# Kernel tuning notes

Measured on AMD Instinct MI355X. Metric: run time of the kernel, lower is better.

## Reference

```python
import jax, jax.numpy as jnp
import numpy as np

B, HIMG, WIMG = 8, 24, 24
WIDTH, NCH, CW = 1024, 8, 128
NHEADS, HD = 8, 16
HALF = HD // 2
NFREQ, VOCAB, NCLS = 32, 256, 10
HIDDEN = 4096
EPS = 1e-6
LAMBDA_INIT = 0.8 - 0.6 * float(np.exp(-0.3 * 0.0))  # layer_idx = 0


def rmsnorm(x, w, eps=EPS):
    return x * jax.lax.rsqrt(jnp.mean(x * x, axis=-1, keepdims=True) + eps) * w


def causal_attn(q, k, v, scale):
    # q,k: [B,H,L,d2], v: [B,H,L,D]
    L = q.shape[2]
    scores = jnp.einsum('bhqd,bhkd->bhqk', q, k) * scale
    mask = jnp.tril(jnp.ones((L, L), dtype=bool))
    scores = jnp.where(mask, scores, -jnp.inf)
    return jnp.einsum('bhqk,bhkd->bhqd', jax.nn.softmax(scores, axis=-1), v)


def diff_attn(h, qkv_w, qkv_b, qn_w, kn_w, hn_w, lq1, lk1, lq2, lk2, ow, ob):
    Bb, L, C = h.shape
    qkv = jax.nn.silu(h @ qkv_w + qkv_b).reshape(Bb, L, 3, NHEADS, HD)
    q, k, v = qkv[:, :, 0], qkv[:, :, 1], qkv[:, :, 2]
    t = lambda a: a.transpose(0, 2, 1, 3)  # [B,L,H,d] -> [B,H,L,d]
    q1 = t(rmsnorm(q[..., :HALF], qn_w)); q2 = t(rmsnorm(q[..., HALF:], qn_w))
    k1 = t(rmsnorm(k[..., :HALF], kn_w)); k2 = t(rmsnorm(k[..., HALF:], kn_w))
    v = t(v)
    lam = jnp.exp(jnp.dot(lq1, lk1)) - jnp.exp(jnp.dot(lq2, lk2)) + LAMBDA_INIT
    scale = 1.0 / np.sqrt(HALF)
    out1 = causal_attn(q1, k1, v, scale)
    out2 = causal_attn(q2, k2, v, scale)
    diff = rmsnorm(out1 - lam * out2, hn_w) * (1.0 - LAMBDA_INIT)
    out = diff.transpose(0, 2, 1, 3).reshape(Bb, L, C)
    return jax.nn.silu(out @ ow + ob)


def setup_inputs() -> dict:
    key = jax.random.key(0)
    ks = iter(jax.random.split(key, 64))
    n = lambda shape, s=0.02: jax.random.normal(next(ks), shape, jnp.float32) * s
    return dict(
        x=jax.random.uniform(next(ks), (B, HIMG, WIMG), jnp.float32),
        top_k=4,
        pixel_embed=n((VOCAB, WIDTH)),
        freq_h=n((NFREQ,), 0.1), freq_w=n((NFREQ,), 0.1),
        phase_h=jnp.zeros((NFREQ,), jnp.float32), phase_w=jnp.zeros((NFREQ,), jnp.float32),
        pos_proj_w=n((4 * NFREQ, WIDTH)), pos_proj_b=jnp.zeros((WIDTH,), jnp.float32),
        embed_norm_w=jnp.ones((WIDTH,), jnp.float32),
        se_w1=n((WIDTH, WIDTH // 4)), se_b1=jnp.zeros((WIDTH // 4,), jnp.float32),
        se_w2=n((WIDTH // 4, WIDTH)), se_b2=jnp.zeros((WIDTH,), jnp.float32),
        mix_norm_w=jnp.ones((WIDTH,), jnp.float32),
        mlp_w1=n((WIDTH, HIDDEN)), mlp_b1=jnp.zeros((HIDDEN,), jnp.float32),
        mlp_w2=n((HIDDEN, WIDTH)), mlp_b2=jnp.zeros((WIDTH,), jnp.float32),
        mlp_norm_w=jnp.ones((WIDTH,), jnp.float32),
        router_w=n((WIDTH, NCH)), router_b=jnp.zeros((NCH,), jnp.float32),
        qkv_w=n((NCH, CW, 3 * CW)), qkv_b=jnp.zeros((NCH, 3 * CW), jnp.float32),
        q_norm_w=jnp.ones((NCH, HALF), jnp.float32), k_norm_w=jnp.ones((NCH, HALF), jnp.float32),
        head_norm_w=jnp.ones((NCH, HD), jnp.float32),
        lam_q1=n((NCH, HALF), 0.1), lam_k1=n((NCH, HALF), 0.1),
        lam_q2=n((NCH, HALF), 0.1), lam_k2=n((NCH, HALF), 0.1),
        out_w=n((NCH, CW, CW)), out_b=jnp.zeros((NCH, CW), jnp.float32),
        seg_norm_w=jnp.ones((NCH, CW), jnp.float32),
        head_w=n((WIDTH, NCLS)), head_b=jnp.zeros((NCLS,), jnp.float32),
    )


def reference(x, top_k, pixel_embed, freq_h, freq_w, phase_h, phase_w, pos_proj_w,
              pos_proj_b, embed_norm_w, se_w1, se_b1, se_w2, se_b2, mix_norm_w,
              mlp_w1, mlp_b1, mlp_w2, mlp_b2, mlp_norm_w, router_w, router_b,
              qkv_w, qkv_b, q_norm_w, k_norm_w, head_norm_w, lam_q1, lam_k1,
              lam_q2, lam_k2, out_w, out_b, seg_norm_w, head_w, head_b):
    Bb, H, W = x.shape
    L = H * W
    # LearnedSinusoidal2DEmbed
    hp = jnp.arange(H, dtype=jnp.float32) / H
    wp = jnp.arange(W, dtype=jnp.float32) / W
    fh = jax.nn.softplus(freq_h) * 10.0
    fw = jax.nn.softplus(freq_w) * 10.0
    ha = hp[:, None] * fh + phase_h          # [H, NFREQ]
    wa = wp[:, None] * fw + phase_w
    h_enc = jnp.concatenate([jnp.sin(ha), jnp.cos(ha)], -1)
    w_enc = jnp.concatenate([jnp.sin(wa), jnp.cos(wa)], -1)
    pos = jnp.concatenate([jnp.broadcast_to(h_enc[:, None], (H, W, 2 * NFREQ)),
                           jnp.broadcast_to(w_enc[None, :], (H, W, 2 * NFREQ))], -1)
    pos = pos @ pos_proj_w + pos_proj_b      # [H, W, WIDTH]
    xi = jnp.clip((x * 255.0).astype(jnp.int32), 0, 255).reshape(Bb, L)
    h = pixel_embed[xi] + pos.reshape(1, L, WIDTH)
    h = rmsnorm(h, embed_norm_w)
    # ChannelMixer: SE + RMSNorm residual, MLP residual, top-k router
    s = jnp.mean(h, axis=1)
    s = jax.nn.sigmoid(jax.nn.silu(s @ se_w1 + se_b1) @ se_w2 + se_b2)
    h = h + rmsnorm(h * s[:, None, :] - h, mix_norm_w)
    h = h + rmsnorm(jax.nn.silu(h @ mlp_w1 + mlp_b1) @ mlp_w2 + mlp_b2, mlp_norm_w)
    logits_r = jnp.mean(h, axis=1) @ router_w + router_b   # [B, NCH]
    tv, ti = jax.lax.top_k(logits_r, top_k)
    rw = jnp.zeros_like(logits_r).at[jnp.arange(Bb)[:, None], ti].set(jax.nn.softmax(tv, axis=-1))
    # ChannelSegment: per-channel differential attention expert, routed
    outs = []
    for i in range(NCH):
        hi = h[..., i * CW:(i + 1) * CW]
        o = diff_attn(hi, qkv_w[i], qkv_b[i], q_norm_w[i], k_norm_w[i], head_norm_w[i],
                      lam_q1[i], lam_k1[i], lam_q2[i], lam_k2[i], out_w[i], out_b[i])
        hi = hi + rmsnorm(o, seg_norm_w[i])
        outs.append(hi * rw[:, i][:, None, None])
    h = jnp.concatenate(outs, axis=-1)
    # classifier head
    return jnp.mean(h, axis=1) @ head_w + head_b
```

## Files before the change

kernel.cpp:

```cpp
#include <hip/hip_runtime.h>
#include <math.h>

typedef __bf16 bf16;
typedef __bf16 bf16x8 __attribute__((ext_vector_type(8)));
typedef __bf16 bf16x4 __attribute__((ext_vector_type(4)));
typedef __bf16 bf16x2 __attribute__((ext_vector_type(2)));
typedef float f32x4 __attribute__((ext_vector_type(4)));
typedef short s16x4 __attribute__((ext_vector_type(4)));

constexpr int Bsz = 8, HIMG = 24, WIMG = 24;
constexpr int Lq = 576;
constexpr int WIDTH = 1024, NCH = 8, CW = 128;
constexpr int NHEADS = 8, HD = 16, HALF = 8;
constexpr float EPS = 1e-6f;
constexpr float LAMINIT = 0.2f;
constexpr float QSCALE_E = 0.35355339059327373f * 1.4426950408889634f;
constexpr int ROWS = Bsz * Lq;
constexpr long PSTRIDE = 4718592;

__device__ __forceinline__ float fexp2(float x) {
#if __has_builtin(__builtin_amdgcn_exp2f)
  return __builtin_amdgcn_exp2f(x);
#else
  return exp2f(x);
#endif
}

constexpr size_t B_HB    = 0;
constexpr size_t B_G2B   = B_HB    + 9437184;
constexpr size_t B_ENCB  = B_G2B   + 9437184;
constexpr size_t B_POSWT = B_ENCB  + 163840;
constexpr size_t B_QKVWT = B_POSWT + 262144;
constexpr size_t B_OWT   = B_QKVWT + 786432;
constexpr size_t B_SE    = B_OWT   + 262144;
constexpr size_t B_T1    = B_SE    + 32768;
constexpr size_t B_MP    = B_T1    + 8192;
constexpr size_t B_RW    = B_MP    + 524288;
constexpr size_t B_LAM   = B_RW    + 256;
constexpr size_t B_POOL  = B_LAM   + 256;
constexpr size_t WS_BIG  = B_POOL + 8388608 + 8388608 + 37748736;
constexpr size_t WS_BIG2 = WS_BIG + 9437184;
constexpr size_t WS_BIG3 = WS_BIG + 4 * 9437184;

__device__ __forceinline__ float blockReduceSum256(float v, float* red) {
  #pragma unroll
  for (int off = 32; off; off >>= 1) v += __shfl_down(v, off, 64);
  int lane = threadIdx.x & 63, wid = threadIdx.x >> 6;
  if (lane == 0) red[wid] = v;
  __syncthreads();
  float total = 0.f;
  #pragma unroll
  for (int i = 0; i < 4; i++) total += red[i];
  return total;
}
__device__ __forceinline__ float silu(float x) { return x / (1.f + __expf(-x)); }

__device__ __forceinline__ void gl16(const bf16* g, bf16* l) {
  __builtin_amdgcn_global_load_lds(
      (const __attribute__((address_space(1))) void*)g,
      (__attribute__((address_space(3))) void*)l, 16, 0, 0);
}

__device__ __forceinline__ f32x4 mfma16(bf16x4 a, bf16x4 b, f32x4 c) {
#if __has_builtin(__builtin_amdgcn_mfma_f32_16x16x16bf16_1k)
  union { bf16x4 h; s16x4 s; } ua, ub;
  ua.h = a; ub.h = b;
  return __builtin_amdgcn_mfma_f32_16x16x16bf16_1k(ua.s, ub.s, c, 0, 0, 0);
#else
  f32x4 d = c;
  asm volatile("v_mfma_f32_16x16x16_bf16 %0, %1, %2, %0"
               : "+v"(d) : "v"(a), "v"(b));
  return d;
#endif
}

__device__ __forceinline__ void tcast_tile(const float* __restrict__ W,
    bf16* __restrict__ Wt, int K, int N, long zo, int bx, int by) {
  __shared__ float t[32][33];
  int n0 = bx * 32, k0 = by * 32;
  int tid = threadIdx.x;
  int r = tid >> 3, c4 = (tid & 7) * 4;
  const float4 v = *(const float4*)(W + zo + (long)(k0 + r) * N + n0 + c4);
  t[c4 + 0][r] = v.x; t[c4 + 1][r] = v.y; t[c4 + 2][r] = v.z; t[c4 + 3][r] = v.w;
  __syncthreads();
  bf16* dst = Wt + zo + (long)(n0 + r) * K + k0 + c4;
  dst[0] = (bf16)t[r][c4 + 0]; dst[1] = (bf16)t[r][c4 + 1];
  dst[2] = (bf16)t[r][c4 + 2]; dst[3] = (bf16)t[r][c4 + 3];
}

__global__ __launch_bounds__(256) void k_tcast_all(
    const float* __restrict__ w1, const float* __restrict__ w2,
    const float* __restrict__ posw, const float* __restrict__ qkvw,
    const float* __restrict__ outw,
    bf16* __restrict__ W1T, bf16* __restrict__ W2T, bf16* __restrict__ POSWT,
    bf16* __restrict__ QKVWT, bf16* __restrict__ OWT) {
  int bid = blockIdx.x;
  if (bid < 4096) {
    tcast_tile(w1, W1T, 1024, 4096, 0, bid % 128, bid / 128);
  } else if (bid < 8192) {
    int t = bid - 4096;
    tcast_tile(w2, W2T, 4096, 1024, 0, t % 32, t / 32);
  } else if (bid < 8320) {
    int t = bid - 8192;
    tcast_tile(posw, POSWT, 128, 1024, 0, t % 32, t / 32);
  } else if (bid < 8704) {
    int t = bid - 8320;
    int z = t / 48; t -= z * 48;
    tcast_tile(qkvw, QKVWT, 128, 384, (long)z * 49152, t % 12, t / 12);
  } else {
    int t = bid - 8704;
    int z = t / 16; t -= z * 16;
    tcast_tile(outw, OWT, 128, 128, (long)z * 16384, t % 4, t / 4);
  }
}

__global__ void k_enc_b(const float* __restrict__ fh, const float* __restrict__ fw,
                        const float* __restrict__ ph, const float* __restrict__ pw,
                        bf16* __restrict__ enc) {
  int idx = blockIdx.x * blockDim.x + threadIdx.x;
  if (idx >= Lq * 128) return;
  int l = idx >> 7, c = idx & 127;
  int hh = l / WIMG, ww = l % WIMG;
  float v;
  if (c < 64) {
    int f = c & 31;
    float fr = log1pf(__expf(fh[f])) * 10.f;
    float a = (hh / (float)HIMG) * fr + ph[f];
    v = (c < 32) ? sinf(a) : cosf(a);
  } else {
    int f = c & 31;
    float fr = log1pf(__expf(fw[f])) * 10.f;
    float a = (ww / (float)WIMG) * fr + pw[f];
    v = (c < 96) ? sinf(a) : cosf(a);
  }
  enc[idx] = (bf16)v;
}

template <int ACT, int OUTBF, int SWZ>
__global__ __launch_bounds__(256) void gemm_bt(
    const bf16* __restrict__ A, int lda, long aZs,
    const bf16* __restrict__ Bt, int ldb, long bZs,
    const float* __restrict__ bias, int biasZs,
    void* __restrict__ Cv, int ldc, long cZs,
    int M, int N, int K) {
  __shared__ bf16 As[128 * 32];
  __shared__ bf16 Bs[128 * 32];
  int tid = threadIdx.x;
  int m0, n0, z;
  if constexpr (SWZ == 0) {
    m0 = blockIdx.y * 128; n0 = blockIdx.x * 128; z = blockIdx.z;
  } else if constexpr (SWZ == 1) {
    int lid = blockIdx.x;
    int xcd = lid & 7, idx = lid >> 3;
    int j = idx & 15, G = xcd + 8 * (idx >> 4);
    m0 = (G % 36) * 128; n0 = ((G / 36) * 16 + j) * 128; z = 0;
  } else {
    int lid = blockIdx.x;
    int xcd = lid & 7, idx = lid >> 3;
    int n = idx & 7, G = xcd + 8 * (idx >> 3);
    m0 = (G % 36) * 128; n0 = n * 128; z = G / 36;
  }
  const bf16* Ab = A + (long)z * aZs;
  const bf16* Bb = Bt + (long)z * bZs;
  f32x4 acc[4][4] = {};
  int wv = tid >> 6, lane = tid & 63;
  int wrow = (wv >> 1) * 64, wcol = (wv & 1) * 64;
  int lm = lane & 15, lq = lane >> 4;
  const bf16* ag = Ab + (long)(m0 + (tid >> 2)) * lda + (tid & 3) * 8;
  const bf16* bg = Bb + (long)(n0 + (tid >> 2)) * ldb + (tid & 3) * 8;
  bf16* asd = As + tid * 8;
  bf16* bsd = Bs + tid * 8;
  for (int k0 = 0; k0 < K; k0 += 32) {
    gl16(ag + k0, asd);
    gl16(ag + k0 + 64L * lda, asd + 2048);
    gl16(bg + k0, bsd);
    gl16(bg + k0 + 64L * ldb, bsd + 2048);
    __syncthreads();
    bf16x8 af[4], bfr[4];
    #pragma unroll
    for (int i = 0; i < 4; i++) {
      af[i]  = *(const bf16x8*)(As + (wrow + i * 16 + lm) * 32 + lq * 8);
      bfr[i] = *(const bf16x8*)(Bs + (wcol + i * 16 + lm) * 32 + lq * 8);
    }
    #pragma unroll
    for (int i = 0; i < 4; i++)
      #pragma unroll
      for (int j = 0; j < 4; j++)
        acc[i][j] = __builtin_amdgcn_mfma_f32_16x16x32_bf16(af[i], bfr[j], acc[i][j], 0, 0, 0);
    __syncthreads();
  }
  long cz = (long)z * cZs;
  const float* bz = bias ? bias + (long)z * biasZs : nullptr;
  #pragma unroll
  for (int i = 0; i < 4; i++) {
    int row = m0 + wrow + i * 16 + lq * 4;
    #pragma unroll
    for (int j = 0; j < 4; j++) {
      int col = n0 + wcol + j * 16 + lm;
      float bv = bz ? bz[col] : 0.f;
      #pragma unroll
      for (int r = 0; r < 4; r++) {
        float v = acc[i][j][r] + bv;
        if (ACT == 1) v = silu(v);
        long off = cz + (long)(row + r) * ldc + col;
        if (OUTBF) ((bf16*)Cv)[off] = (bf16)v;
        else       ((float*)Cv)[off] = v;
      }
    }
  }
}

template <int ACT>
__global__ __launch_bounds__(512) void gemm256(
    const bf16* __restrict__ A, int lda, long aZs,
    const bf16* __restrict__ Bt, int ldb, long bZs,
    const float* __restrict__ bias,
    bf16* __restrict__ C, int ldc, long cZs,
    int Mtiles, int Ntiles, int K) {
  __shared__ bf16 LDS[65536];
  const int tid = threadIdx.x;
  const int cpx = gridDim.x >> 3;
  const int wg = (blockIdx.x & 7) * cpx + (blockIdx.x >> 3);
  const int per_z = Mtiles * Ntiles;
  const int z = wg / per_z, rwg = wg % per_z;
  const int m0 = (rwg / Ntiles) * 256, n0 = (rwg % Ntiles) * 256;
  const bf16* Ab = A + (long)z * aZs;
  const bf16* Bb = Bt + (long)z * bZs;
  const int c0 = tid, c1 = tid + 512;
  const int sr0 = c0 >> 3, sc0 = ((c0 & 7) ^ (sr0 & 7)) * 8;
  const int sr1 = c1 >> 3, sc1 = ((c1 & 7) ^ (sr1 & 7)) * 8;
  const long a00 = (long)(m0 + sr0) * lda + sc0;
  const long a01 = (long)(m0 + sr1) * lda + sc1;
  const long a10 = (long)(m0 + 128 + sr0) * lda + sc0;
  const long a11 = (long)(m0 + 128 + sr1) * lda + sc1;
  const long b00 = (long)(n0 + sr0) * ldb + sc0;
  const long b01 = (long)(n0 + sr1) * ldb + sc1;
  const long b10 = (long)(n0 + 128 + sr0) * ldb + sc0;
  const long b11 = (long)(n0 + 128 + sr1) * ldb + sc1;
  const int d0 = c0 * 8, d1 = c1 * 8;
  auto stage = [&](int kt, int buf) {
    const bf16* Ak = Ab + kt * 64;
    const bf16* Bk = Bb + kt * 64;
    bf16* L = LDS + buf * 32768;
    gl16(Ak + a00, L + d0);         gl16(Ak + a01, L + d1);
    gl16(Ak + a10, L + 8192 + d0);  gl16(Ak + a11, L + 8192 + d1);
    gl16(Bk + b00, L + 16384 + d0); gl16(Bk + b01, L + 16384 + d1);
    gl16(Bk + b10, L + 24576 + d0); gl16(Bk + b11, L + 24576 + d1);
  };
  const int wv = tid >> 6, lane = tid & 63;
  const int wm = wv >> 2, wn = wv & 3;
  const int lm = lane & 15, lq = lane >> 4;
  const int sw = lm & 7;
  const int abase = wm * 8192;
  const int bbase = 16384 + (wn >> 1) * 8192;
  const int brow0 = (wn & 1) * 64;
  const int kq0 = (lq ^ sw) * 8;
  const int kq1 = ((4 + lq) ^ sw) * 8;
  f32x4 acc[8][4] = {};
  bf16x8 afr[4][2], bfr[2][2];
  const int NT = K >> 6;
  stage(0, 0);
  asm volatile("s_waitcnt vmcnt(0)" ::: "memory");
  __builtin_amdgcn_s_barrier();
  for (int s = 0; s < NT; ++s) {
    const int bb = (s & 1) * 32768;
    const bf16* La = LDS + bb + abase + lm * 64;
    const bf16* Lb = LDS + bb + bbase + (brow0 + lm) * 64;
    #pragma unroll
    for (int f = 0; f < 4; f++) {
      afr[f][0] = *(const bf16x8*)(La + f * 1024 + kq0);
      afr[f][1] = *(const bf16x8*)(La + f * 1024 + kq1);
    }
    #pragma unroll
    for (int g = 0; g < 2; g++) {
      bfr[g][0] = *(const bf16x8*)(Lb + g * 1024 + kq0);
      bfr[g][1] = *(const bf16x8*)(Lb + g * 1024 + kq1);
    }
    if (s + 1 < NT) stage(s + 1, ((s & 1) ^ 1));
    __builtin_amdgcn_s_barrier();
    __builtin_amdgcn_s_setprio(1);
    #pragma unroll
    for (int f = 0; f < 4; f++)
      #pragma unroll
      for (int g = 0; g < 2; g++) {
        acc[f][g] = __builtin_amdgcn_mfma_f32_16x16x32_bf16(afr[f][0], bfr[g][0], acc[f][g], 0, 0, 0);
        acc[f][g] = __builtin_amdgcn_mfma_f32_16x16x32_bf16(afr[f][1], bfr[g][1], acc[f][g], 0, 0, 0);
      }
    __builtin_amdgcn_s_setprio(0);
    __builtin_amdgcn_s_barrier();
    #pragma unroll
    for (int g = 0; g < 2; g++) {
      bfr[g][0] = *(const bf16x8*)(Lb + 2048 + g * 1024 + kq0);
      bfr[g][1] = *(const bf16x8*)(Lb + 2048 + g * 1024 + kq1);
    }
    __builtin_amdgcn_s_barrier();
    __builtin_amdgcn_s_setprio(1);
    #pragma unroll
    for (int f = 0; f < 4; f++)
      #pragma unroll
      for (int g = 0; g < 2; g++) {
        acc[f][2 + g] = __builtin_amdgcn_mfma_f32_16x16x32_bf16(afr[f][0], bfr[g][0], acc[f][2 + g], 0, 0, 0);
        acc[f][2 + g] = __builtin_amdgcn_mfma_f32_16x16x32_bf16(afr[f][1], bfr[g][1], acc[f][2 + g], 0, 0, 0);
      }
    __builtin_amdgcn_s_setprio(0);
    __builtin_amdgcn_s_barrier();
    #pragma unroll
    for (int f = 0; f < 4; f++) {
      afr[f][0] = *(const bf16x8*)(La + 4096 + f * 1024 + kq0);
      afr[f][1] = *(const bf16x8*)(La + 4096 + f * 1024 + kq1);
    }
    __builtin_amdgcn_s_barrier();
    __builtin_amdgcn_s_setprio(1);
    #pragma unroll
    for (int f = 0; f < 4; f++)
      #pragma unroll
      for (int g = 0; g < 2; g++) {
        acc[4 + f][2 + g] = __builtin_amdgcn_mfma_f32_16x16x32_bf16(afr[f][0], bfr[g][0], acc[4 + f][2 + g], 0, 0, 0);
        acc[4 + f][2 + g] = __builtin_amdgcn_mfma_f32_16x16x32_bf16(afr[f][1], bfr[g][1], acc[4 + f][2 + g], 0, 0, 0);
      }
    __builtin_amdgcn_s_setprio(0);
    __builtin_amdgcn_s_barrier();
    #pragma unroll
    for (int g = 0; g < 2; g++) {
      bfr[g][0] = *(const bf16x8*)(Lb + g * 1024 + kq0);
      bfr[g][1] = *(const bf16x8*)(Lb + g * 1024 + kq1);
    }
    __builtin_amdgcn_s_barrier();
    __builtin_amdgcn_s_setprio(1);
    #pragma unroll
    for (int f = 0; f < 4; f++)
      #pragma unroll
      for (int g = 0; g < 2; g++) {
        acc[4 + f][g] = __builtin_amdgcn_mfma_f32_16x16x32_bf16(afr[f][0], bfr[g][0], acc[4 + f][g], 0, 0, 0);
        acc[4 + f][g] = __builtin_amdgcn_mfma_f32_16x16x32_bf16(afr[f][1], bfr[g][1], acc[4 + f][g], 0, 0, 0);
      }
    __builtin_amdgcn_s_setprio(0);
    if (s + 1 < NT) { asm volatile("s_waitcnt vmcnt(0)" ::: "memory"); }
    __builtin_amdgcn_s_barrier();
  }
  const long cz = (long)z * cZs;
  #pragma unroll
  for (int i = 0; i < 8; i++) {
    const int row = m0 + wm * 128 + (i >> 2) * 64 + (i & 3) * 16 + lq * 4;
    #pragma unroll
    for (int j = 0; j < 4; j++) {
      const int col = n0 + wn * 64 + (j >> 1) * 32 + (j & 1) * 16 + lm;
      const float bv = bias ? bias[col] : 0.f;
      #pragma unroll
      for (int rr = 0; rr < 4; rr++) {
        float v = acc[i][j][rr] + bv;
        if (ACT == 1) v = silu(v);
        C[cz + (long)(row + rr) * ldc + col] = (bf16)v;
      }
    }
  }
}

template <int ACT, int OUTBF, int ACC, int NORM>
__global__ __launch_bounds__(256) void gemm64(
    const bf16* __restrict__ A, int lda, long aZs,
    const bf16* __restrict__ Bt, int ldb, long bZs,
    const float* __restrict__ bias, int biasZs,
    void* __restrict__ Cv, int ldc, long cZs,
    int M, int N, int K,
    const float* __restrict__ qn, const float* __restrict__ kn) {
  __shared__ bf16 As[64 * 32];
  __shared__ bf16 Bs[128 * 32];
  int tid = threadIdx.x;
  int m0 = blockIdx.y * 64, n0 = blockIdx.x * 128;
  int z = blockIdx.z;
  const bf16* Ab = A + (long)z * aZs;
  const bf16* Bb = Bt + (long)z * bZs;
  f32x4 acc[4][2] = {};
  int wv = tid >> 6, lane = tid & 63;
  int lm = lane & 15, lq = lane >> 4;
  int wcol = wv * 32;
  const bf16* ag = Ab + (long)(m0 + (tid >> 2)) * lda + (tid & 3) * 8;
  const bf16* bg = Bb + (long)(n0 + (tid >> 2)) * ldb + (tid & 3) * 8;
  bf16* asd = As + tid * 8;
  bf16* bsd = Bs + tid * 8;
  for (int k0 = 0; k0 < K; k0 += 32) {
    gl16(ag + k0, asd);
    gl16(bg + k0, bsd);
    gl16(bg + k0 + 64L * ldb, bsd + 2048);
    __syncthreads();
    bf16x8 af[4], bfr[2];
    #pragma unroll
    for (int i = 0; i < 4; i++)
      af[i] = *(const bf16x8*)(As + (i * 16 + lm) * 32 + lq * 8);
    #pragma unroll
    for (int j = 0; j < 2; j++)
      bfr[j] = *(const bf16x8*)(Bs + (wcol + j * 16 + lm) * 32 + lq * 8);
    #pragma unroll
    for (int i = 0; i < 4; i++)
      #pragma unroll
      for (int j = 0; j < 2; j++)
        acc[i][j] = __builtin_amdgcn_mfma_f32_16x16x32_bf16(af[i], bfr[j], acc[i][j], 0, 0, 0);
    __syncthreads();
  }
  long cz = (long)z * cZs;
  const float* bz = bias ? bias + (long)z * biasZs : nullptr;
  if constexpr (NORM == 0) {
    #pragma unroll
    for (int i = 0; i < 4; i++) {
      int row = m0 + i * 16 + lq * 4;
      #pragma unroll
      for (int j = 0; j < 2; j++) {
        int col = n0 + wcol + j * 16 + lm;
        float bv = bz ? bz[col] : 0.f;
        #pragma unroll
        for (int r = 0; r < 4; r++) {
          float v = acc[i][j][r] + bv;
          long off = cz + (long)(row + r) * ldc + col;
          if (ACC) v += (float)((bf16*)Cv)[off];
          if (ACT == 1) v = silu(v);
          if (OUTBF) ((bf16*)Cv)[off] = (bf16)v;
          else       ((float*)Cv)[off] = v;
        }
      }
    }
  } else {
    int nsec = blockIdx.x;
    bool don = nsec < 2;
    float wnv = 1.f;
    if (nsec == 0) wnv = qn[z * 8 + (lm & 7)] * QSCALE_E;
    else if (nsec == 1) wnv = kn[z * 8 + (lm & 7)];
    #pragma unroll
    for (int i = 0; i < 4; i++) {
      int row = m0 + i * 16 + lq * 4;
      #pragma unroll
      for (int j = 0; j < 2; j++) {
        int col = n0 + wcol + j * 16 + lm;
        float bv = bz ? bz[col] : 0.f;
        #pragma unroll
        for (int r = 0; r < 4; r++) {
          float v = acc[i][j][r] + bv;
          if (ACT == 1) v = silu(v);
          float s = v * v;
          s += __shfl_xor(s, 1);
          s += __shfl_xor(s, 2);
          s += __shfl_xor(s, 4);
          if (don) v = v * rsqrtf(s * 0.125f + EPS) * wnv;
          ((bf16*)Cv)[cz + (long)(row + r) * ldc + col] = (bf16)v;
        }
      }
    }
  }
}

__global__ __launch_bounds__(256) void k_embed(const float* __restrict__ x,
    const float* __restrict__ emb, const float* __restrict__ pos,
    const float* __restrict__ nw, bf16* __restrict__ h) {
  __shared__ float red[4];
  int row = blockIdx.x;
  int l = row % Lq;
  int xi = (int)(x[row] * 255.f);
  xi = min(max(xi, 0), 255);
  const float* er = emb + (long)xi * WIDTH;
  const float* pr = pos + (long)l * WIDTH;
  int c0 = threadIdx.x * 4;
  float v[4]; float ss = 0.f;
  #pragma unroll
  for (int i = 0; i < 4; i++) { v[i] = er[c0 + i] + pr[c0 + i]; ss += v[i] * v[i]; }
  ss = blockReduceSum256(ss, red);
  float r = rsqrtf(ss / WIDTH + EPS);
  bf16* hr = h + (long)row * WIDTH;
  #pragma unroll
  for (int i = 0; i < 4; i++) hr[c0 + i] = (bf16)(v[i] * r * nw[c0 + i]);
}

__global__ void k_meanl_p(const bf16* __restrict__ h, float* __restrict__ part) {
  int lp = blockIdx.x, b = blockIdx.y, t = threadIdx.x;
  const bf16* p = h + ((long)b * Lq + (long)lp * 36) * WIDTH + t * 4;
  float a0 = 0, a1 = 0, a2 = 0, a3 = 0;
  for (int l = 0; l < 36; l++) {
    bf16x4 v = *(const bf16x4*)(p + (long)l * WIDTH);
    a0 += (float)v[0]; a1 += (float)v[1]; a2 += (float)v[2]; a3 += (float)v[3];
  }
  float* dst = part + ((long)b * 16 + lp) * WIDTH + t * 4;
  dst[0] = a0; dst[1] = a1; dst[2] = a2; dst[3] = a3;
}

__global__ __launch_bounds__(256) void k_se1(const float* __restrict__ part,
    const float* __restrict__ w1, const float* __restrict__ b1,
    float* __restrict__ t1) {
  __shared__ float sv[1024];
  __shared__ float red[256];
  int jb = blockIdx.x, b = blockIdx.y, t = threadIdx.x;
  for (int c = t; c < 1024; c += 256) {
    float a = 0.f;
    #pragma unroll
    for (int lp = 0; lp < 16; lp++) a += part[((long)b * 16 + lp) * 1024 + c];
    sv[c] = a * (1.f / 576.f);
  }
  __syncthreads();
  int j = t & 7, pt = t >> 3;
  int j0 = jb * 8;
  float acc = 0.f;
  int c0 = pt * 32;
  #pragma unroll 8
  for (int c = c0; c < c0 + 32; c++) acc += sv[c] * w1[c * 256 + j0 + j];
  red[t] = acc;
  __syncthreads();
  if (t < 8) {
    float a = b1[j0 + t];
    #pragma unroll
    for (int p = 0; p < 32; p++) a += red[p * 8 + t];
    t1[b * 256 + j0 + t] = silu(a);
  }
}

__global__ __launch_bounds__(256) void k_se2(const float* __restrict__ t1,
    const float* __restrict__ w2, const float* __restrict__ b2,
    float* __restrict__ s) {
  __shared__ float red[256];
  int jb = blockIdx.x, b = blockIdx.y, t = threadIdx.x;
  int j = t & 31, pt = t >> 5;
  int j0 = jb * 32;
  const float* tb = t1 + b * 256;
  float acc = 0.f;
  int c0 = pt * 32;
  #pragma unroll 8
  for (int c = c0; c < c0 + 32; c++) acc += tb[c] * w2[c * 1024 + j0 + j];
  red[t] = acc;
  __syncthreads();
  if (t < 32) {
    float a = b2[j0 + t];
    #pragma unroll
    for (int p = 0; p < 8; p++) a += red[p * 32 + t];
    s[b * 1024 + j0 + t] = 1.f / (1.f + __expf(-a));
  }
}

__global__ __launch_bounds__(256) void k_mix_b(bf16* __restrict__ h,
    const float* __restrict__ s, const float* __restrict__ mw) {
  __shared__ float red[4];
  int row = blockIdx.x;
  int b = row / Lq;
  bf16* hr = h + (long)row * WIDTH;
  const float* sb = s + b * WIDTH;
  int c0 = threadIdx.x * 4;
  float hv[4], y[4]; float ss = 0.f;
  #pragma unroll
  for (int i = 0; i < 4; i++) {
    hv[i] = (float)hr[c0 + i];
    y[i] = hv[i] * (sb[c0 + i] - 1.f); ss += y[i] * y[i];
  }
  ss = blockReduceSum256(ss, red);
  float r = rsqrtf(ss / WIDTH + EPS);
  #pragma unroll
  for (int i = 0; i < 4; i++) hr[c0 + i] = (bf16)(hv[i] + y[i] * r * mw[c0 + i]);
}

__global__ __launch_bounds__(256) void k_addnorm_b(bf16* __restrict__ h,
    const bf16* __restrict__ g, const float* __restrict__ mw) {
  __shared__ float red[4];
  int row = blockIdx.x;
  bf16* hr = h + (long)row * WIDTH;
  const bf16* gr = g + (long)row * WIDTH;
  int c0 = threadIdx.x * 4;
  float y[4]; float ss = 0.f;
  #pragma unroll
  for (int i = 0; i < 4; i++) { y[i] = (float)gr[c0 + i]; ss += y[i] * y[i]; }
  ss = blockReduceSum256(ss, red);
  float r = rsqrtf(ss / WIDTH + EPS);
  #pragma unroll
  for (int i = 0; i < 4; i++)
    hr[c0 + i] = (bf16)((float)hr[c0 + i] + y[i] * r * mw[c0 + i]);
}

__global__ __launch_bounds__(256) void k_addnorm2(bf16* __restrict__ h,
    const bf16* __restrict__ p0, const bf16* __restrict__ p1,
    const float* __restrict__ b2, const float* __restrict__ mw) {
  __shared__ float red[4];
  int row = blockIdx.x;
  bf16* hr = h + (long)row * WIDTH;
  const bf16* g0 = p0 + (long)row * WIDTH;
  const bf16* g1 = p1 + (long)row * WIDTH;
  int c0 = threadIdx.x * 4;
  float y[4]; float ss = 0.f;
  #pragma unroll
  for (int i = 0; i < 4; i++) {
    y[i] = (float)g0[c0 + i] + (float)g1[c0 + i] + b2[c0 + i];
    ss += y[i] * y[i];
  }
  ss = blockReduceSum256(ss, red);
  float r = rsqrtf(ss / WIDTH + EPS);
  #pragma unroll
  for (int i = 0; i < 4; i++)
    hr[c0 + i] = (bf16)((float)hr[c0 + i] + y[i] * r * mw[c0 + i]);
}

__global__ __launch_bounds__(256) void k_addnorm4(bf16* __restrict__ h,
    const bf16* __restrict__ parts, const float* __restrict__ b2,
    const float* __restrict__ mw) {
  __shared__ float red[4];
  int row = blockIdx.x;
  bf16* hr = h + (long)row * WIDTH;
  const bf16* g0 = parts + (long)row * WIDTH;
  int c0 = threadIdx.x * 4;
  float y[4]; float ss = 0.f;
  #pragma unroll
  for (int i = 0; i < 4; i++) {
    float a = b2[c0 + i];
    #pragma unroll
    for (int p = 0; p < 4; p++) a += (float)g0[(long)p * PSTRIDE + c0 + i];
    y[i] = a; ss += a * a;
  }
  ss = blockReduceSum256(ss, red);
  float r = rsqrtf(ss / WIDTH + EPS);
  #pragma unroll
  for (int i = 0; i < 4; i++)
    hr[c0 + i] = (bf16)((float)hr[c0 + i] + y[i] * r * mw[c0 + i]);
}

__global__ __launch_bounds__(256) void k_router(const float* __restrict__ part,
    const float* __restrict__ rwgt, const float* __restrict__ rb,
    const float* __restrict__ lq1, const float* __restrict__ lk1,
    const float* __restrict__ lq2, const float* __restrict__ lk2,
    float* __restrict__ rw, float* __restrict__ lam) {
  __shared__ float sv[1024];
  __shared__ float red[256];
  __shared__ float lg[8];
  int b = blockIdx.x, t = threadIdx.x;
  for (int c = t; c < 1024; c += 256) {
    float a = 0.f;
    #pragma unroll
    for (int lp = 0; lp < 16; lp++) a += part[((long)b * 16 + lp) * 1024 + c];
    sv[c] = a * (1.f / 576.f);
  }
  __syncthreads();
  int j = t & 7, pt = t >> 3;
  float acc = 0.f;
  int c0 = pt * 32;
  #pragma unroll 8
  for (int c = c0; c < c0 + 32; c++) acc += sv[c] * rwgt[c * 8 + j];
  red[t] = acc;
  __syncthreads();
  if (t < 8) {
    float a = rb[t];
    for (int p = 0; p < 32; p++) a += red[p * 8 + t];
    lg[t] = a;
  }
  __syncthreads();
  if (t == 0) {
    float v[8]; bool sel[8];
    #pragma unroll
    for (int i = 0; i < 8; i++) { v[i] = lg[i]; sel[i] = false; }
    int idxs[4]; float vals[4];
    for (int s = 0; s < 4; s++) {
      int bi = -1; float bv = -1e30f;
      for (int i = 0; i < 8; i++) if (!sel[i] && v[i] > bv) { bv = v[i]; bi = i; }
      sel[bi] = true; idxs[s] = bi; vals[s] = bv;
    }
    float m = vals[0], den = 0.f, e[4];
    for (int s = 0; s < 4; s++) { e[s] = __expf(vals[s] - m); den += e[s]; }
    for (int i = 0; i < 8; i++) rw[b * 8 + i] = 0.f;
    for (int s = 0; s < 4; s++) rw[b * 8 + idxs[s]] = e[s] / den;
  }
  if (b == 0 && t >= 8 && t < 16) {
    int c = t - 8;
    float d1 = 0.f, d2 = 0.f;
    for (int i = 0; i < 8; i++) {
      d1 += lq1[c * 8 + i] * lk1[c * 8 + i];
      d2 += lq2[c * 8 + i] * lk2[c * 8 + i];
    }
    lam[c] = __expf(d1) - __expf(d2) + LAMINIT;
  }
}

__global__ __launch_bounds__(256) void k_attn_mfma(
    const bf16* __restrict__ qkv, const float* __restrict__ lam,
    const float* __restrict__ hnw, bf16* __restrict__ dc) {
  __shared__ bf16 Ks[576 * 16];
  __shared__ bf16 Vt[16 * 584];
  int tid = threadIdx.x;
  int slice = blockIdx.x; int zc = slice >> 3, b = slice & 7;
  int head = blockIdx.z;
  const bf16* qkvb = qkv + ((long)zc * ROWS + (long)b * Lq) * 384;
  for (int i = tid; i < 1152; i += 256) {
    int row = i >> 1, hf = i & 1;
    gl16(qkvb + (long)row * 384 + 128 + head * 16 + hf * 8, Ks + i * 8);
  }
  for (int i = tid; i < 1152; i += 256) {
    int row = i >> 1, dh = i & 1;
    bf16x8 v = *(const bf16x8*)(qkvb + (long)row * 384 + 256 + head * 16 + dh * 8);
    #pragma unroll
    for (int j = 0; j < 8; j++) Vt[(dh * 8 + j) * 584 + row] = v[j];
  }
  __syncthreads();
  int wv = tid >> 6, lane = tid & 63;
  int lm = lane & 15, lq = lane >> 4;
  float lamv = lam[zc];
  float hwv[4];
  #pragma unroll
  for (int r = 0; r < 4; r++) hwv[r] = hnw[zc * 16 + lq * 4 + r] * (1.f - LAMINIT);
  int u = blockIdx.y * 4 + wv;
  int prA, prB, prC;
  if (u < 6) { prA = u + 2; prB = 17 - u; prC = -1; }
  else       { int v2 = u - 6; prA = v2; prB = 8 + v2; prC = 11 - v2; }
  for (int pi = 0; pi < 3; pi++) {
    int pr = (pi == 0) ? prA : (pi == 1) ? prB : prC;
    if (pr < 0) continue;
    bf16x8 bq0[2] = {{}, {}}, bq1[2] = {{}, {}};
    if (lq < 2) {
      #pragma unroll
      for (int tile = 0; tile < 2; tile++) {
        bf16x8 t8 = *(const bf16x8*)(
            qkvb + (long)(pr * 32 + tile * 16 + lm) * 384 + head * 16 + lq * 8);
        if (lq == 0) bq0[tile] = t8; else bq1[tile] = t8;
      }
    }
    f32x4 o[2][2] = {};
    float den[2][2] = {};
    for (int kc = 0; kc <= pr; kc++) {
      f32x4 sT[2][2][2] = {};
      #pragma unroll
      for (int t = 0; t < 2; t++) {
        bf16x8 aK = {};
        if (lq < 2) aK = *(const bf16x8*)(Ks + (kc * 32 + t * 16 + lm) * 16 + lq * 8);
        #pragma unroll
        for (int tile = 0; tile < 2; tile++) {
          sT[t][tile][0] = __builtin_amdgcn_mfma_f32_16x16x32_bf16(aK, bq0[tile], sT[t][tile][0], 0, 0, 0);
          sT[t][tile][1] = __builtin_amdgcn_mfma_f32_16x16x32_bf16(aK, bq1[tile], sT[t][tile][1], 0, 0, 0);
        }
      }
      bool diag = (kc == pr);
      #pragma unroll
      for (int t = 0; t < 2; t++) {
        bf16x4 aV = *(const bf16x4*)(Vt + lm * 584 + kc * 32 + t * 16 + lq * 4);
        #pragma unroll
        for (int tile = 0; tile < 2; tile++) {
          if (diag && tile == 0 && t == 1) continue;
          bool masked = diag && (tile == t);
          #pragma unroll
          for (int h2 = 0; h2 < 2; h2++) {
            bf16x4 pb;
            float dsum = 0.f;
            #pragma unroll
            for (int r = 0; r < 4; r++) {
              float ev = fexp2(sT[t][tile][h2][r]);
              if (masked && (lq * 4 + r > lm)) ev = 0.f;
              dsum += ev;
              pb[r] = (bf16)ev;
            }
            den[tile][h2] += dsum;
            o[tile][h2] = mfma16(aV, pb, o[tile][h2]);
          }
        }
      }
    }
    #pragma unroll
    for (int tile = 0; tile < 2; tile++)
      #pragma unroll
      for (int h2 = 0; h2 < 2; h2++) {
        den[tile][h2] += __shfl_xor(den[tile][h2], 16);
        den[tile][h2] += __shfl_xor(den[tile][h2], 32);
      }
    #pragma unroll
    for (int tile = 0; tile < 2; tile++) {
      float inv1 = 1.f / den[tile][0];
      float inv2 = lamv / den[tile][1];
      float dff[4]; float ss = 0.f;
      #pragma unroll
      for (int r = 0; r < 4; r++) {
        dff[r] = o[tile][0][r] * inv1 - o[tile][1][r] * inv2;
        ss += dff[r] * dff[r];
      }
      ss += __shfl_xor(ss, 16);
      ss += __shfl_xor(ss, 32);
      float rr = rsqrtf(ss * 0.0625f + EPS);
      bf16x4 outp;
      #pragma unroll
      for (int r = 0; r < 4; r++) outp[r] = (bf16)(dff[r] * rr * hwv[r]);
      long rowg = (long)zc * ROWS + (long)b * Lq + pr * 32 + tile * 16 + lm;
      *(bf16x4*)(dc + rowg * 128 + head * 16 + lq * 4) = outp;
    }
  }
}

__global__ __launch_bounds__(64) void k_segpool(const bf16* __restrict__ h,
    const bf16* __restrict__ op, const float* __restrict__ segw,
    const float* __restrict__ rw, float* __restrict__ part) {
  int lp = blockIdx.x, b = blockIdx.y, ch = blockIdx.z;
  int t = threadIdx.x;
  int c0 = t * 2;
  float w0 = segw[ch * 128 + c0], w1 = segw[ch * 128 + c0 + 1];
  float rwv = rw[b * 8 + ch];
  float a0 = 0.f, a1 = 0.f;
  for (int l = 0; l < 36; l++) {
    int row = b * Lq + lp * 36 + l;
    const bf16* oprow = op + (long)ch * ROWS * CW + (long)row * CW;
    bf16x2 yv = *(const bf16x2*)(oprow + c0);
    float y0 = (float)yv[0], y1 = (float)yv[1];
    float ss = y0 * y0 + y1 * y1;
    #pragma unroll
    for (int m = 1; m < 64; m <<= 1) ss += __shfl_xor(ss, m);
    float r = rsqrtf(ss * (1.f / 128.f) + EPS);
    bf16x2 hv = *(const bf16x2*)(h + (long)row * WIDTH + ch * 128 + c0);
    a0 += ((float)hv[0] + y0 * r * w0) * rwv;
    a1 += ((float)hv[1] + y1 * r * w1) * rwv;
  }
  float* dst = part + ((long)b * 16 + lp) * 1024 + ch * 128 + c0;
  dst[0] = a0; dst[1] = a1;
}

__global__ __launch_bounds__(256) void k_head(const float* __restrict__ part,
    const float* __restrict__ hw, const float* __restrict__ hb, float* __restrict__ out) {
  __shared__ float pool[1024];
  __shared__ float red[256];
  int b = blockIdx.x, t = threadIdx.x;
  for (int c = t; c < 1024; c += 256) {
    float a = 0.f;
    #pragma unroll
    for (int lp = 0; lp < 16; lp++) a += part[((long)b * 16 + lp) * 1024 + c];
    pool[c] = a * (1.f / 576.f);
  }
  __syncthreads();
  int j = t & 15, pt = t >> 4;
  float acc = 0.f;
  if (j < 10)
    for (int c = pt * 64; c < pt * 64 + 64; c++)
      acc += pool[c] * hw[c * 10 + j];
  red[t] = acc;
  __syncthreads();
  if (t < 10) {
    float a = hb[t];
    for (int p = 0; p < 16; p++) a += red[p * 16 + t];
    out[b * 10 + t] = a;
  }
}

extern "C" void kernel_launch(void* const* d_in, const int* in_sizes, int n_in,
                              void* d_out, int out_size, void* d_ws, size_t ws_size,
                              hipStream_t stream) {
  const float* x          = (const float*)d_in[0];
  const float* pixel_embed= (const float*)d_in[2];
  const float* freq_h     = (const float*)d_in[3];
  const float* freq_w     = (const float*)d_in[4];
  const float* phase_h    = (const float*)d_in[5];
  const float* phase_w    = (const float*)d_in[6];
  const float* pos_proj_w = (const float*)d_in[7];
  const float* pos_proj_b = (const float*)d_in[8];
  const float* embed_norm = (const float*)d_in[9];
  const float* se_w1      = (const float*)d_in[10];
  const float* se_b1      = (const float*)d_in[11];
  const float* se_w2      = (const float*)d_in[12];
  const float* se_b2      = (const float*)d_in[13];
  const float* mix_norm   = (const float*)d_in[14];
  const float* mlp_w1     = (const float*)d_in[15];
  const float* mlp_b1     = (const float*)d_in[16];
  const float* mlp_w2     = (const float*)d_in[17];
  const float* mlp_b2     = (const float*)d_in[18];
  const float* mlp_norm   = (const float*)d_in[19];
  const float* router_w   = (const float*)d_in[20];
  const float* router_b   = (const float*)d_in[21];
  const float* qkv_w      = (const float*)d_in[22];
  const float* qkv_b      = (const float*)d_in[23];
  const float* q_norm_w   = (const float*)d_in[24];
  const float* k_norm_w   = (const float*)d_in[25];
  const float* head_norm_w= (const float*)d_in[26];
  const float* lam_q1     = (const float*)d_in[27];
  const float* lam_k1     = (const float*)d_in[28];
  const float* lam_q2     = (const float*)d_in[29];
  const float* lam_k2     = (const float*)d_in[30];
  const float* out_w      = (const float*)d_in[31];
  const float* out_b      = (const float*)d_in[32];
  const float* seg_norm_w = (const float*)d_in[33];
  const float* head_w     = (const float*)d_in[34];
  const float* head_b     = (const float*)d_in[35];

  char* W = (char*)d_ws;
  bf16*  HB    = (bf16*)(W + B_HB);
  bf16*  G2B   = (bf16*)(W + B_G2B);
  float* POS   = (float*)(W + B_G2B);
  bf16*  ENCB  = (bf16*)(W + B_ENCB);
  bf16*  POSWT = (bf16*)(W + B_POSWT);
  bf16*  QKVWT = (bf16*)(W + B_QKVWT);
  bf16*  OWT   = (bf16*)(W + B_OWT);
  float* SE    = (float*)(W + B_SE);
  float* T1    = (float*)(W + B_T1);
  float* MP    = (float*)(W + B_MP);
  float* RW    = (float*)(W + B_RW);
  float* LAM   = (float*)(W + B_LAM);
  char*  P     = W + B_POOL;
  bf16*  W1T   = (bf16*)P;
  bf16*  W2T   = (bf16*)(P + 8388608);
  bf16*  HID   = (bf16*)(P + 16777216);
  bf16*  PARTS = (bf16*)(P + 16777216 + 37748736);
  bf16*  QKV   = (bf16*)P;
  bf16*  DC    = (bf16*)(P + 28311552);
  float* out   = (float*)d_out;
  const int tier = (ws_size >= WS_BIG3) ? 3 : (ws_size >= WS_BIG2) ? 2
                 : (ws_size >= WS_BIG) ? 1 : 0;

  k_tcast_all<<<8832, 256, 0, stream>>>(mlp_w1, mlp_w2, pos_proj_w, qkv_w, out_w,
                                        W1T, W2T, POSWT, QKVWT, OWT);
  k_enc_b<<<288, 256, 0, stream>>>(freq_h, freq_w, phase_h, phase_w, ENCB);
  gemm64<0, 0, 0, 0><<<dim3(8, 10, 1), 256, 0, stream>>>(
      ENCB, 128, 0, POSWT, 128, 0, pos_proj_b, 0, POS, 1024, 0, 640, 1024, 128,
      nullptr, nullptr);
  k_embed<<<ROWS, 256, 0, stream>>>(x, pixel_embed, POS, embed_norm, HB);
  k_meanl_p<<<dim3(16, 8), 256, 0, stream>>>(HB, MP);
  k_se1<<<dim3(32, 8), 256, 0, stream>>>(MP, se_w1, se_b1, T1);
  k_se2<<<dim3(32, 8), 256, 0, stream>>>(T1, se_w2, se_b2, SE);
  k_mix_b<<<ROWS, 256, 0, stream>>>(HB, SE, mix_norm);
  if (tier >= 1) {
    gemm256<1><<<256, 512, 0, stream>>>(
        HB, 1024, 0, W1T, 1024, 0, mlp_b1,
        HID, 4096, 0, 16, 16, 1024);
    gemm_bt<1, 1, 0><<<dim3(32, 4, 1), 256, 0, stream>>>(
        HB + 4096L * 1024, 1024, 0, W1T, 1024, 0, mlp_b1, 0,
        HID + 4096L * 4096, 4096, 0, 512, 4096, 1024);
    if (tier == 3) {
      gemm256<0><<<256, 512, 0, stream>>>(
          HID, 4096, 1024, W2T, 4096, 1024, nullptr,
          PARTS, 1024, PSTRIDE, 16, 4, 1024);
      gemm_bt<0, 1, 0><<<dim3(8, 4, 4), 256, 0, stream>>>(
          HID + 4096L * 4096, 4096, 1024, W2T, 4096, 1024, nullptr, 0,
          PARTS + 4096L * 1024, 1024, PSTRIDE, 512, 1024, 1024);
      k_addnorm4<<<ROWS, 256, 0, stream>>>(HB, PARTS, mlp_b2, mlp_norm);
    } else if (tier == 2) {
      gemm_bt<0, 1, 2><<<576, 256, 0, stream>>>(
          HID, 4096, 2048, W2T, 4096, 2048, nullptr, 0,
          G2B, 1024, (long)(PARTS - G2B), 4608, 1024, 2048);
      k_addnorm2<<<ROWS, 256, 0, stream>>>(HB, G2B, PARTS, mlp_b2, mlp_norm);
    } else {
      gemm64<0, 1, 0, 0><<<dim3(8, 72, 1), 256, 0, stream>>>(
          HID, 4096, 0, W2T, 4096, 0, mlp_b2, 0,
          G2B, 1024, 0, 4608, 1024, 4096, nullptr, nullptr);
      k_addnorm_b<<<ROWS, 256, 0, stream>>>(HB, G2B, mlp_norm);
    }
  } else {
    gemm_bt<1, 1, 0><<<dim3(16, 36, 1), 256, 0, stream>>>(
        HB, 1024, 0, W1T, 1024, 0, mlp_b1, 0, HID, 2048, 0, 4608, 2048, 1024);
    gemm64<0, 1, 0, 0><<<dim3(8, 72, 1), 256, 0, stream>>>(
        HID, 2048, 0, W2T, 4096, 0, mlp_b2, 0, G2B, 1024, 0, 4608, 1024, 2048,
        nullptr, nullptr);
    gemm_bt<1, 1, 0><<<dim3(16, 36, 1), 256, 0, stream>>>(
        HB, 1024, 0, W1T + 2048L * 1024, 1024, 0, mlp_b1 + 2048, 0, HID, 2048, 0,
        4608, 2048, 1024);
    gemm64<0, 1, 1, 0><<<dim3(8, 72, 1), 256, 0, stream>>>(
        HID, 2048, 0, W2T + 2048, 4096, 0, nullptr, 0, G2B, 1024, 0,
        4608, 1024, 2048, nullptr, nullptr);
    k_addnorm_b<<<ROWS, 256, 0, stream>>>(HB, G2B, mlp_norm);
  }
  k_meanl_p<<<dim3(16, 8), 256, 0, stream>>>(HB, MP);
  k_router<<<8, 256, 0, stream>>>(MP, router_w, router_b,
                                  lam_q1, lam_k1, lam_q2, lam_k2, RW, LAM);
  gemm64<1, 1, 0, 1><<<dim3(3, 72, 8), 256, 0, stream>>>(
      HB, 1024, CW, QKVWT, 128, 384 * 128, qkv_b, 384,
      QKV, 384, (long)ROWS * 384, ROWS, 384, 128, q_norm_w, k_norm_w);
  k_attn_mfma<<<dim3(64, 2, 8), 256, 0, stream>>>(QKV, LAM, head_norm_w, DC);
  gemm64<1, 1, 0, 0><<<dim3(1, 72, 8), 256, 0, stream>>>(
      DC, 128, (long)ROWS * 128, OWT, 128, 128 * 128, out_b, 128,
      DC, 128, (long)ROWS * 128, ROWS, 128, 128, nullptr, nullptr);
  k_segpool<<<dim3(16, 8, 8), 64, 0, stream>>>(HB, DC, seg_norm_w, RW, MP);
  k_head<<<8, 256, 0, stream>>>(MP, head_w, head_b, out);
}
```

Before: 451.6 us.

## Vectorize transpose store, change GEMM LDS swizzle, compute softmax denominators via MFMA

Three unrelated changes. The weight transpose-cast kernel now writes four bf16 values with one vector store instead of four scalar stores. The GEMM LDS swizzle is reduced from an XOR with row&7 to a single bit taken from row bit 2, which changes the bank-conflict pattern of both the async global-to-LDS stores and the fragment reads. In the attention kernel, softmax denominators are accumulated by an extra MFMA against a ones vector rather than by scalar adds and cross-lane shuffles, trading VALU and shuffle work for additional matrix instructions.

```diff
diff --git a/kernel.cpp b/kernel.cpp
--- a/kernel.cpp
+++ b/kernel.cpp
@@ -84,8 +84,10 @@
   t[c4 + 0][r] = v.x; t[c4 + 1][r] = v.y; t[c4 + 2][r] = v.z; t[c4 + 3][r] = v.w;
   __syncthreads();
   bf16* dst = Wt + zo + (long)(n0 + r) * K + k0 + c4;
-  dst[0] = (bf16)t[r][c4 + 0]; dst[1] = (bf16)t[r][c4 + 1];
-  dst[2] = (bf16)t[r][c4 + 2]; dst[3] = (bf16)t[r][c4 + 3];
+  bf16x4 o4;
+  o4[0] = (bf16)t[r][c4 + 0]; o4[1] = (bf16)t[r][c4 + 1];
+  o4[2] = (bf16)t[r][c4 + 2]; o4[3] = (bf16)t[r][c4 + 3];
+  *(bf16x4*)dst = o4;
 }
 
 __global__ __launch_bounds__(256) void k_tcast_all(
@@ -227,8 +229,8 @@
   const bf16* Ab = A + (long)z * aZs;
   const bf16* Bb = Bt + (long)z * bZs;
   const int c0 = tid, c1 = tid + 512;
-  const int sr0 = c0 >> 3, sc0 = ((c0 & 7) ^ (sr0 & 7)) * 8;
-  const int sr1 = c1 >> 3, sc1 = ((c1 & 7) ^ (sr1 & 7)) * 8;
+  const int sr0 = c0 >> 3, sc0 = ((c0 & 7) ^ (((sr0 >> 2) & 1) << 1)) * 8;
+  const int sr1 = c1 >> 3, sc1 = ((c1 & 7) ^ (((sr1 >> 2) & 1) << 1)) * 8;
   const long a00 = (long)(m0 + sr0) * lda + sc0;
   const long a01 = (long)(m0 + sr1) * lda + sc1;
   const long a10 = (long)(m0 + 128 + sr0) * lda + sc0;
@@ -250,12 +252,12 @@
   const int wv = tid >> 6, lane = tid & 63;
   const int wm = wv >> 2, wn = wv & 3;
   const int lm = lane & 15, lq = lane >> 4;
-  const int sw = lm & 7;
+  const int swb = ((lm >> 2) & 1) << 1;
   const int abase = wm * 8192;
   const int bbase = 16384 + (wn >> 1) * 8192;
   const int brow0 = (wn & 1) * 64;
-  const int kq0 = (lq ^ sw) * 8;
-  const int kq1 = ((4 + lq) ^ sw) * 8;
+  const int kq0 = (lq ^ swb) * 8;
+  const int kq1 = ((4 + lq) ^ swb) * 8;
   f32x4 acc[8][4] = {};
   bf16x8 afr[4][2], bfr[2][2];
   const int NT = K >> 6;
@@ -695,6 +697,8 @@
   float hwv[4];
   #pragma unroll
   for (int r = 0; r < 4; r++) hwv[r] = hnw[zc * 16 + lq * 4 + r] * (1.f - LAMINIT);
+  const bf16 one = (bf16)1.0f;
+  const bf16x4 ONES = {one, one, one, one};
   int u = blockIdx.y * 4 + wv;
   int prA, prB, prC;
   if (u < 6) { prA = u + 2; prB = 17 - u; prC = -1; }
@@ -712,7 +716,7 @@
       }
     }
     f32x4 o[2][2] = {};
-    float den[2][2] = {};
+    f32x4 dacc[2][2] = {};
     for (int kc = 0; kc <= pr; kc++) {
       f32x4 sT[2][2][2] = {};
       #pragma unroll
@@ -736,31 +740,22 @@
           #pragma unroll
           for (int h2 = 0; h2 < 2; h2++) {
             bf16x4 pb;
-            float dsum = 0.f;
             #pragma unroll
             for (int r = 0; r < 4; r++) {
               float ev = fexp2(sT[t][tile][h2][r]);
               if (masked && (lq * 4 + r > lm)) ev = 0.f;
-              dsum += ev;
               pb[r] = (bf16)ev;
             }
-            den[tile][h2] += dsum;
+            dacc[tile][h2] = mfma16(ONES, pb, dacc[tile][h2]);
             o[tile][h2] = mfma16(aV, pb, o[tile][h2]);
           }
         }
       }
     }
     #pragma unroll
-    for (int tile = 0; tile < 2; tile++)
-      #pragma unroll
-      for (int h2 = 0; h2 < 2; h2++) {
-        den[tile][h2] += __shfl_xor(den[tile][h2], 16);
-        den[tile][h2] += __shfl_xor(den[tile][h2], 32);
-      }
-    #pragma unroll
     for (int tile = 0; tile < 2; tile++) {
-      float inv1 = 1.f / den[tile][0];
-      float inv2 = lamv / den[tile][1];
+      float inv1 = 1.f / dacc[tile][0][0];
+      float inv2 = lamv / dacc[tile][1][0];
       float dff[4]; float ss = 0.f;
       #pragma unroll
       for (int r = 0; r < 4; r++) {
```

Result: no change. 456.2 us (+1.0%).
